# Kernel tuning notes

Hardware: AMD Instinct MI355X
Metric: run time of the kernel (lower is better)

## Reference

```python
import jax, jax.numpy as jnp
import numpy as np

B, IN, U = 16, 1024, 1024


def _wSw(W, S):
    # W: [i,u], S: [b,i,i] -> W^T S W : [b,u,u]
    return jnp.einsum('iu,bij,jv->buv', W, S, W)


def _xSx(x, Wsig):
    # (sum_i x_i^2) * W_Sigma, broadcast over batch
    return jnp.sum(x * x, axis=1)[:, None, None] * Wsig


def _trS(S, Wsig):
    return jnp.trace(S, axis1=1, axis2=2)[:, None, None] * Wsig


def _hadamard_sigma(s1, s2, m1, m2):
    # s1*s2 + diag(m1) s2 diag(m1) + diag(m2) s1 diag(m2)
    return (s1 * s2
            + m1[:, :, None] * s2 * m1[:, None, :]
            + m2[:, :, None] * s1 * m2[:, None, :])


def _act_sigma(g, S):
    # S * outer(g, g)
    return S * (g[:, :, None] * g[:, None, :])


def setup_inputs() -> dict:
    key = jax.random.key(0)
    ks = jax.random.split(key, 16)
    f32 = jnp.float32
    init_mu, ini_sigma = 0.05, -4.6
    inp = {
        'mu_inputs': jax.random.normal(ks[0], (B, IN), f32),
        'sigma_inputs': 0.01 * jax.random.normal(ks[1], (B, IN, IN), f32),
        'prev_state': 0.1 * jax.random.normal(ks[2], (B, U), f32),
        'Sigma_state': 0.01 * jax.random.normal(ks[3], (B, U, U), f32),
        'U_z': init_mu * jax.random.normal(ks[4], (IN, U), f32),
        'uz_sigma': jnp.full((U,), ini_sigma, f32),
        'W_z': init_mu * jax.random.normal(ks[5], (U, U), f32),
        'wz_sigma': jnp.full((U,), ini_sigma, f32),
        'U_r': init_mu * jax.random.normal(ks[6], (IN, U), f32),
        'ur_sigma': jnp.full((U,), ini_sigma, f32),
        'W_r': init_mu * jax.random.normal(ks[7], (U, U), f32),
        'wr_sigma': jnp.full((U,), ini_sigma, f32),
        'U_h': init_mu * jax.random.normal(ks[8], (IN, U), f32),
        'uh_sigma': jnp.full((U,), ini_sigma, f32),
        'W_h': init_mu * jax.random.normal(ks[9], (U, U), f32),
        'wh_sigma': jnp.full((U,), ini_sigma, f32),
    }
    return inp


def reference(mu_inputs, sigma_inputs, prev_state, Sigma_state,
              U_z, uz_sigma, W_z, wz_sigma,
              U_r, ur_sigma, W_r, wr_sigma,
              U_h, uh_sigma, W_h, wh_sigma):
    sp = jax.nn.softplus
    # ---- z gate ----
    pre_z = mu_inputs @ U_z + prev_state @ W_z
    z = jax.nn.sigmoid(pre_z)
    Uz_S, Wz_S = jnp.diag(sp(uz_sigma)), jnp.diag(sp(wz_sigma))
    Sigma_zz = (_wSw(U_z, sigma_inputs) + _xSx(mu_inputs, Uz_S) + _trS(sigma_inputs, Uz_S)
                + _wSw(W_z, Sigma_state) + _xSx(prev_state, Wz_S) + _trS(Sigma_state, Wz_S))
    Sigma_z = _act_sigma(z * (1.0 - z), Sigma_zz)  # analytic d sigmoid
    # ---- r gate ----
    pre_r = mu_inputs @ U_r + prev_state @ W_r
    r = jax.nn.sigmoid(pre_r)
    Ur_S, Wr_S = jnp.diag(sp(ur_sigma)), jnp.diag(sp(wr_sigma))
    Sigma_rr = (_wSw(U_r, sigma_inputs) + _xSx(mu_inputs, Ur_S) + _trS(sigma_inputs, Ur_S)
                + _wSw(W_r, Sigma_state) + _xSx(prev_state, Wr_S) + _trS(Sigma_state, Wr_S))
    Sigma_r = _act_sigma(r * (1.0 - r), Sigma_rr)
    # ---- h gate ----
    sr = prev_state * r
    pre_h = mu_inputs @ U_h + sr @ W_h
    h = jnp.tanh(pre_h)
    Uh_S, Wh_S = jnp.diag(sp(uh_sigma)), jnp.diag(sp(wh_sigma))
    sigma_g = _hadamard_sigma(Sigma_state, Sigma_r, prev_state, r)
    Sigma_hh = (_wSw(U_h, sigma_inputs) + _xSx(mu_inputs, Uh_S) + _trS(sigma_inputs, Uh_S)
                + _wSw(W_h, sigma_g) + _xSx(sr, Wh_S) + _trS(sigma_g, Wh_S))
    Sigma_h = _act_sigma(1.0 - h * h, Sigma_hh)  # analytic d tanh
    # ---- combine ----
    mu_out = z * prev_state + (1.0 - z) * h
    sigma_a = _hadamard_sigma(Sigma_z, Sigma_state, z, prev_state)
    sigma_b = _hadamard_sigma(Sigma_z, Sigma_h, 1.0 - z, h)
    sigma_ab = Sigma_z * (prev_state[:, :, None] * h[:, None, :])
    sigma_abT = Sigma_z * (h[:, :, None] * prev_state[:, None, :])
    Sigma_out = sigma_a + sigma_b - sigma_ab - sigma_abT
    Sigma_out = jnp.where(jnp.isfinite(Sigma_out), Sigma_out, jnp.zeros_like(Sigma_out))
    eye = jnp.eye(Sigma_out.shape[-1], dtype=bool)
    Sigma_out = jnp.where(eye, jnp.abs(Sigma_out), Sigma_out)
    return mu_out, Sigma_out
```

## Files before the change

### kernel.cpp

```cpp
#include <hip/hip_runtime.h>
#include <math.h>


#define B_  16
#define N_  1024
#define NN_ (1024*1024)

typedef __bf16 bf16x8 __attribute__((ext_vector_type(8)));
typedef float  f32x4  __attribute__((ext_vector_type(4)));
typedef unsigned short ushort8v __attribute__((ext_vector_type(8)));

__device__ __forceinline__ unsigned short f2bf(float f) {
  union { float f; unsigned int u; } v; v.f = f;
  unsigned int r = v.u + 0x7fffu + ((v.u >> 16) & 1u);
  return (unsigned short)(r >> 16);
}
__device__ __forceinline__ float bf2f(unsigned short h) {
  union { unsigned int u; float f; } v; v.u = ((unsigned int)h) << 16;
  return v.f;
}
__device__ __forceinline__ float f4get(const float4& v, int q) {
  return q == 0 ? v.x : (q == 1 ? v.y : (q == 2 ? v.z : v.w));
}
__device__ __forceinline__ unsigned short u4get(const ushort4& v, int q) {
  return q == 0 ? v.x : (q == 1 ? v.y : (q == 2 ? v.z : v.w));
}

__device__ __forceinline__ void gload_lds16(const void* g, void* l) {
  __builtin_amdgcn_global_load_lds((__attribute__((address_space(1))) void*)g,
                                   (__attribute__((address_space(3))) void*)l,
                                   16, 0, 0);
}

#define MFMA_ __builtin_amdgcn_mfma_f32_16x16x32_bf16
#define SBAR_()  do { __builtin_amdgcn_sched_barrier(0); \
                      __builtin_amdgcn_s_barrier(); \
                      __builtin_amdgcn_sched_barrier(0); } while (0)

template<int OMODE, int PAIR>
__global__ __launch_bounds__(512)
void gemm8p(const unsigned short* __restrict__ A, int lda, long aStride, int koffA,
            const unsigned short* __restrict__ Bm, const unsigned short* __restrict__ Bm2,
            int ldb, long bStride, int K,
            void* __restrict__ Out, int ldo, long oStride, int noff,
            const float* __restrict__ act,
            const float* __restrict__ spU, const float* __restrict__ spW,
            const float* __restrict__ dU, const float* __restrict__ dW)
{
  __shared__ __align__(16) char ldsb[131072];
  const int id = blockIdx.x;
  const int xcd = id & 7, rest = id >> 3;
  const int mt = rest & 3, pp = rest >> 2;
  const int panel = xcd + (pp << 3);
  const int nt = panel & 3;
  const int b  = (panel >> 2) & 15;
  const int ps = PAIR ? (panel >> 6) : 0;
  const unsigned short* Bsel = (PAIR && ps) ? Bm2 : Bm;
  const int kofx = koffA + (ps ? 1024 : 0);
  const int nofx = noff  + (ps ? 1024 : 0);
  const int mbase = mt << 8, nbase = nt << 8;
  const int tid = threadIdx.x, lane = tid & 63, w = tid >> 6;
  const int wm = w >> 2, wn = w & 3;
  const int NT = K >> 6;

  f32x4 acc[8][4];
  const f32x4 zero4 = {0.f, 0.f, 0.f, 0.f};
#pragma unroll
  for (int i = 0; i < 8; i++)
#pragma unroll
    for (int j = 0; j < 4; j++) acc[i][j] = zero4;

  const int l3 = lane >> 3, l7 = lane & 7;
  const int posg = l7 ^ l3;
  const int gr = (l3 << 1) + (posg >> 2);
  const int gc = (posg & 3) << 3;
  const int bi0 = w << 1, bi1 = bi0 + 1;
  const int rS0 = ((bi0 >> 1) << 4) + gr, cS0 = ((bi0 & 1) << 5) + gc;
  const int rS1 = ((bi1 >> 1) << 4) + gr, cS1 = ((bi1 & 1) << 5) + gc;
  const unsigned short* Ab = A + (size_t)b * aStride + (size_t)mbase * lda + kofx;
  const unsigned short* Bb = Bsel + (size_t)b * bStride + (size_t)nbase * ldb;
  const int d0 = w << 11, d1 = (w << 11) + 1024;

  auto SA = [&](int tt, int h) {
    char* dst = ldsb + ((tt & 1) << 16) + (h << 14);
    const unsigned short* s = Ab + (size_t)(h << 7) * lda + ((size_t)tt << 6);
    gload_lds16(s + (size_t)rS0 * lda + cS0, dst + d0);
    gload_lds16(s + (size_t)rS1 * lda + cS1, dst + d1);
  };
  auto SB = [&](int tt, int h) {
    char* dst = ldsb + ((tt & 1) << 16) + 32768 + (h << 14);
    const unsigned short* s = Bb + (size_t)(h << 7) * ldb + ((size_t)tt << 6);
    gload_lds16(s + (size_t)rS0 * ldb + cS0, dst + d0);
    gload_lds16(s + (size_t)rS1 * ldb + cS1, dst + d1);
  };

  const int lrow = lane & 15, c4 = lane >> 4;
  const int aoff = ((lrow >> 1) << 7) + (((((lrow & 1) << 2) | c4) ^ (lrow >> 1)) << 4);
  const int abase = wm << 14;
  const int bbase = 32768 + ((wn >> 1) << 14);
  const int brg   = (wn & 1) << 2;
  auto LDA = [&](const char* pb, int mi, int ks) -> bf16x8 {
    return *(const bf16x8*)(pb + abase + (((mi << 1) + ks) << 10) + aoff);
  };
  auto LDB = [&](const char* pb, int ni, int ks) -> bf16x8 {
    return *(const bf16x8*)(pb + bbase + ((((brg + ni) << 1) + ks) << 10) + aoff);
  };

  SA(0, 0); SA(0, 1); SB(0, 0); SB(0, 1);
  if (NT > 1) { SB(1, 0); SB(1, 1); }
  asm volatile("s_waitcnt vmcnt(4)" ::: "memory");
  SBAR_();

  bf16x8 avA[4], avB[4], bvA[4], bvB[4];
#pragma unroll
  for (int i = 0; i < 4; i++) avB[i] = LDA(ldsb, i, 0);
#pragma unroll
  for (int i = 0; i < 4; i++) bvB[i] = LDB(ldsb, i, 0);
  __builtin_amdgcn_sched_barrier(0);

  for (int kt = 0; kt < NT; ++kt) {
    const char* pb = ldsb + ((kt & 1) << 16);
    const char* pn = ldsb + (((kt + 1) & 1) << 16);
#pragma unroll
    for (int i = 0; i < 4; i++) avA[i] = LDA(pb, 4 + i, 0);
    if (kt + 1 < NT) SA(kt + 1, 0);
    SBAR_();
    __builtin_amdgcn_s_setprio(1);
#pragma unroll
    for (int ni = 0; ni < 4; ni++)
#pragma unroll
      for (int mi = 0; mi < 4; mi++)
        acc[mi][ni] = MFMA_(avB[mi], bvB[ni], acc[mi][ni], 0, 0, 0);
    __builtin_amdgcn_s_setprio(0);
    SBAR_();
#pragma unroll
    for (int i = 0; i < 4; i++) avB[i] = LDA(pb, i, 1);
#pragma unroll
    for (int i = 0; i < 4; i++) bvA[i] = LDB(pb, i, 1);
    if (kt + 1 < NT) SA(kt + 1, 1);
    SBAR_();
    __builtin_amdgcn_s_setprio(1);
#pragma unroll
    for (int ni = 0; ni < 4; ni++)
#pragma unroll
      for (int mi = 0; mi < 4; mi++)
        acc[4 + mi][ni] = MFMA_(avA[mi], bvB[ni], acc[4 + mi][ni], 0, 0, 0);
    __builtin_amdgcn_s_setprio(0);
    SBAR_();
#pragma unroll
    for (int i = 0; i < 4; i++) avA[i] = LDA(pb, 4 + i, 1);
    SBAR_();
    __builtin_amdgcn_s_setprio(1);
#pragma unroll
    for (int ni = 0; ni < 4; ni++)
#pragma unroll
      for (int mi = 0; mi < 4; mi++)
        acc[mi][ni] = MFMA_(avB[mi], bvA[ni], acc[mi][ni], 0, 0, 0);
    __builtin_amdgcn_s_setprio(0);
    SBAR_();
    if (kt + 2 < NT) {
      SB(kt + 2, 0); SB(kt + 2, 1);
      asm volatile("s_waitcnt vmcnt(4)" ::: "memory");
    } else if (kt + 1 < NT) {
      asm volatile("s_waitcnt vmcnt(0)" ::: "memory");
    }
    SBAR_();
    if (kt + 1 < NT) {
#pragma unroll
      for (int i = 0; i < 4; i++) avB[i] = LDA(pn, i, 0);
#pragma unroll
      for (int i = 0; i < 4; i++) bvB[i] = LDB(pn, i, 0);
    }
    __builtin_amdgcn_sched_barrier(0);
    __builtin_amdgcn_s_setprio(1);
#pragma unroll
    for (int ni = 0; ni < 4; ni++)
#pragma unroll
      for (int mi = 0; mi < 4; mi++)
        acc[4 + mi][ni] = MFMA_(avA[mi], bvA[ni], acc[4 + mi][ni], 0, 0, 0);
    __builtin_amdgcn_s_setprio(0);
    SBAR_();
  }

  if (OMODE == 2) {
    const float* actb = act + b * N_;
    const float dUb = dU[b], dWb = dW[b];
#pragma unroll
    for (int mi = 0; mi < 8; mi++) {
      const int u0 = mbase + wm * 128 + mi * 16 + ((lane >> 4) << 2);
#pragma unroll
      for (int ni = 0; ni < 4; ni++) {
        const int v = nbase + wn * 64 + ni * 16 + (lane & 15);
        const float avv = actb[v];
#pragma unroll
        for (int r = 0; r < 4; r++) {
          const int u = u0 + r;
          float val = acc[mi][ni][r];
          if (u == v) val += dUb * spU[u] + dWb * spW[u];
          val *= actb[u] * avv;
          ((float*)Out)[(size_t)b * oStride + (size_t)u * ldo + v] = val;
        }
      }
    }
  } else {
    __syncthreads();
    unsigned short* scr = (unsigned short*)(ldsb + w * 16384);
    const float* actb = (OMODE == 1) ? (act + b * N_) : nullptr;
    float dUb = 0.f, dWb = 0.f;
    if (OMODE == 1) { dUb = dU[b]; dWb = dW[b]; }
#pragma unroll
    for (int mi = 0; mi < 8; mi++) {
      const int rl0 = mi * 16 + ((lane >> 4) << 2);
#pragma unroll
      for (int ni = 0; ni < 4; ni++) {
        const int cl = ni * 16 + (lane & 15);
#pragma unroll
        for (int r = 0; r < 4; r++) {
          const int rl = rl0 + r;
          float val = acc[mi][ni][r];
          if (OMODE == 1) {
            const int u = mbase + wm * 128 + rl, v = nbase + wn * 64 + cl;
            if (u == v) val += dUb * spU[u] + dWb * spW[u];
            val *= actb[u] * actb[v];
          }
          scr[rl * 64 + ((((cl >> 3) ^ (rl & 7))) << 3) + (cl & 7)] = f2bf(val);
        }
      }
    }
    asm volatile("s_waitcnt lgkmcnt(0)" ::: "memory");
    __builtin_amdgcn_sched_barrier(0);
    unsigned short* ob = (unsigned short*)Out + (size_t)b * oStride
        + (size_t)(mbase + wm * 128) * ldo + nofx + nbase + wn * 64;
#pragma unroll
    for (int pq = 0; pq < 16; pq++) {
      const int row = pq * 8 + (lane >> 3);
      const int ch = (lane & 7) ^ (row & 7);
      ushort8v vv = *(const ushort8v*)&scr[row * 64 + ((lane & 7) << 3)];
      *(ushort8v*)(ob + (size_t)row * ldo + ch * 8) = vv;
    }
  }
}


__global__ void conv_bf16(const float* __restrict__ in, unsigned short* __restrict__ out, int n4)
{
  int i = blockIdx.x * 256 + threadIdx.x;
  const int stride = gridDim.x * 256;
  for (; i < n4; i += stride) {
    const float4 v = ((const float4*)in)[i];
    ushort4 o;
    o.x = f2bf(v.x); o.y = f2bf(v.y); o.z = f2bf(v.z); o.w = f2bf(v.w);
    ((ushort4*)out)[i] = o;
  }
}

__global__ void build_AT(const float* __restrict__ Uz, const float* __restrict__ Wz,
                         const float* __restrict__ Ur, const float* __restrict__ Wr,
                         const float* __restrict__ Uh, const float* __restrict__ Wh,
                         unsigned short* __restrict__ AT)
{
  __shared__ float tile[32][33];
  const int g = blockIdx.z;
  const float* U = g == 0 ? Uz : (g == 1 ? Ur : Uh);
  const float* W = g == 0 ? Wz : (g == 1 ? Wr : Wh);
  const int u0  = blockIdx.x * 32;
  const int k0g = blockIdx.y * 32;
  const float* src = (k0g >= 1024) ? W : U;
  const int kloc = k0g & 1023;
  const int tx = threadIdx.x & 31, ty = threadIdx.x >> 5;
  unsigned short* out = AT + (size_t)g * N_ * 2048;
#pragma unroll
  for (int i = 0; i < 32; i += 8) tile[ty + i][tx] = src[(size_t)(kloc + ty + i) * N_ + u0 + tx];
  __syncthreads();
#pragma unroll
  for (int i = 0; i < 32; i += 8)
    out[(size_t)(u0 + ty + i) * 2048 + k0g + tx] = f2bf(tile[tx][ty + i]);
}

__global__ void softplus6(const float* a0, const float* a1, const float* a2,
                          const float* a3, const float* a4, const float* a5,
                          float* __restrict__ sp)
{
  const float* src[6] = {a0, a1, a2, a3, a4, a5};
  const int g = blockIdx.x;
  const float* s = src[g];
  for (int i = threadIdx.x; i < N_; i += 256) {
    float x = s[i];
    sp[g * N_ + i] = (x > 20.f) ? x : log1pf(expf(x));
  }
}

__global__ void scalars1(const float* __restrict__ mu, const float* __restrict__ prev,
                         const float* __restrict__ sin_, const float* __restrict__ Sst,
                         float* __restrict__ dA, float* __restrict__ dBzr)
{
  __shared__ float red[256];
  const int b = blockIdx.x;
  float s1 = 0.f, s2 = 0.f;
  for (int i = threadIdx.x; i < N_; i += 256) {
    const float m = mu[b * N_ + i];
    s1 += m * m + sin_[(size_t)b * NN_ + (size_t)i * (N_ + 1)];
    const float p = prev[b * N_ + i];
    s2 += p * p + Sst[(size_t)b * NN_ + (size_t)i * (N_ + 1)];
  }
  red[threadIdx.x] = s1; __syncthreads();
  for (int s = 128; s > 0; s >>= 1) { if (threadIdx.x < s) red[threadIdx.x] += red[threadIdx.x + s]; __syncthreads(); }
  if (threadIdx.x == 0) dA[b] = red[0];
  __syncthreads();
  red[threadIdx.x] = s2; __syncthreads();
  for (int s = 128; s > 0; s >>= 1) { if (threadIdx.x < s) red[threadIdx.x] += red[threadIdx.x + s]; __syncthreads(); }
  if (threadIdx.x == 0) dBzr[b] = red[0];
}

__global__ __launch_bounds__(256)
void gate_pre2(const float* __restrict__ x1, const float* __restrict__ x2,
               const float* __restrict__ U0, const float* __restrict__ W0,
               const float* __restrict__ U1, const float* __restrict__ W1,
               float* __restrict__ Ppart)
{
  const int g  = blockIdx.z;
  const int ks = blockIdx.y;
  const int out = blockIdx.x * 256 + threadIdx.x;
  const int b = out >> 10, col = out & 1023;
  const float* x = (ks < 4) ? x1 : x2;
  const float* Wm = (g == 0) ? ((ks < 4) ? U0 : W0) : ((ks < 4) ? U1 : W1);
  const int k0 = (ks & 3) * 256;
  const float* xb = x + b * N_ + k0;
  const float* wp = Wm + (size_t)k0 * N_ + col;
  float acc = 0.f;
#pragma unroll 8
  for (int k = 0; k < 256; k++)
    acc += xb[k] * wp[(size_t)k * N_];
  Ppart[(g * 8 + ks) * (B_ * N_) + out] = acc;
}

__global__ void gate_act2(const float* __restrict__ P,
                          float* __restrict__ z, float* __restrict__ gz,
                          float* __restrict__ r, float* __restrict__ gr)
{
  const int out = blockIdx.x * 256 + threadIdx.x;
  float a0 = 0.f, a1 = 0.f;
#pragma unroll
  for (int ks = 0; ks < 8; ks++) {
    a0 += P[ks * (B_ * N_) + out];
    a1 += P[(8 + ks) * (B_ * N_) + out];
  }
  const float s0 = 1.f / (1.f + expf(-a0));
  const float s1 = 1.f / (1.f + expf(-a1));
  z[out] = s0; gz[out] = s0 * (1.f - s0);
  r[out] = s1; gr[out] = s1 * (1.f - s1);
}

__global__ __launch_bounds__(256)
void gate_pre1(const float* __restrict__ x1, const float* __restrict__ x2,
               const float* __restrict__ U0, const float* __restrict__ W0,
               float* __restrict__ Ppart)
{
  const int ks = blockIdx.y;
  const int out = blockIdx.x * 256 + threadIdx.x;
  const int b = out >> 10, col = out & 1023;
  const float* x = (ks < 4) ? x1 : x2;
  const float* Wm = (ks < 4) ? U0 : W0;
  const int k0 = (ks & 3) * 256;
  const float* xb = x + b * N_ + k0;
  const float* wp = Wm + (size_t)k0 * N_ + col;
  float acc = 0.f;
#pragma unroll 8
  for (int k = 0; k < 256; k++)
    acc += xb[k] * wp[(size_t)k * N_];
  Ppart[ks * (B_ * N_) + out] = acc;
}

__global__ void gate_act1(const float* __restrict__ P,
                          float* __restrict__ h, float* __restrict__ gh)
{
  const int out = blockIdx.x * 256 + threadIdx.x;
  float a0 = 0.f;
#pragma unroll
  for (int ks = 0; ks < 8; ks++) a0 += P[ks * (B_ * N_) + out];
  const float s = tanhf(a0);
  h[out] = s; gh[out] = 1.f - s * s;
}

__global__ void sr_csr(const float* __restrict__ prev, const float* __restrict__ r,
                       float* __restrict__ sr, float* __restrict__ csr)
{
  __shared__ float red[256];
  const int b = blockIdx.x;
  float s = 0.f;
  for (int i = threadIdx.x; i < N_; i += 256) {
    const float v = prev[b * N_ + i] * r[b * N_ + i];
    sr[b * N_ + i] = v;
    s += v * v;
  }
  red[threadIdx.x] = s; __syncthreads();
  for (int k = 128; k > 0; k >>= 1) { if (threadIdx.x < k) red[threadIdx.x] += red[threadIdx.x + k]; __syncthreads(); }
  if (threadIdx.x == 0) csr[b] = red[0];
}

__global__ void hadamard_sg(const float* __restrict__ Sst, unsigned short* __restrict__ Sg,
                            const float* __restrict__ prev, const float* __restrict__ r)
{
  const size_t idx = ((size_t)blockIdx.x * 256 + threadIdx.x) * 4;
  const int b = (int)(idx >> 20);
  const int rem = (int)(idx & (NN_ - 1));
  const int i = rem >> 10, j0 = rem & 1023;
  const float pi = prev[b * N_ + i], ri = r[b * N_ + i];
  const float4  ss  = *(const float4*)(Sst + (size_t)b * NN_ + rem);
  const ushort4 sr4 = *(const ushort4*)(Sg + (size_t)b * NN_ + rem);
  ushort4 o;
  unsigned short* op = (unsigned short*)&o;
#pragma unroll
  for (int q = 0; q < 4; q++) {
    const float srv = bf2f(u4get(sr4, q));
    const float stv = f4get(ss, q);
    const float pj = prev[b * N_ + j0 + q];
    const float rj = r[b * N_ + j0 + q];
    op[q] = f2bf(stv * srv + pi * pj * srv + ri * rj * stv);
  }
  *(ushort4*)(Sg + (size_t)b * NN_ + rem) = o;
}

__global__ void scalars2(const unsigned short* __restrict__ Sg,
                         const float* __restrict__ csr, float* __restrict__ dBh)
{
  __shared__ float red[256];
  const int b = blockIdx.x;
  float s = 0.f;
  for (int i = threadIdx.x; i < N_; i += 256)
    s += bf2f(Sg[(size_t)b * NN_ + (size_t)i * (N_ + 1)]);
  red[threadIdx.x] = s; __syncthreads();
  for (int k = 128; k > 0; k >>= 1) { if (threadIdx.x < k) red[threadIdx.x] += red[threadIdx.x + k]; __syncthreads(); }
  if (threadIdx.x == 0) dBh[b] = red[0] + csr[b];
}

__global__ void mu_kernel(const float* __restrict__ z, const float* __restrict__ prev,
                          const float* __restrict__ h, float* __restrict__ mu_out)
{
  const int i = blockIdx.x * 256 + threadIdx.x;
  const float zz = z[i];
  mu_out[i] = zz * prev[i] + (1.f - zz) * h[i];
}

__global__ void combine(const unsigned short* __restrict__ Sz, const float* __restrict__ Sst,
                        const float* __restrict__ z, const float* __restrict__ prev,
                        const float* __restrict__ h, float* __restrict__ SigOut)
{
  const int row = blockIdx.x;
  const int b = row >> 10, u = row & 1023;
  const float zu = z[b * N_ + u], pu = prev[b * N_ + u], hu = h[b * N_ + u];
  const size_t base = (size_t)b * NN_ + (size_t)u * N_;
  const int j0 = threadIdx.x * 4;
  const ushort4 s4 = *(const ushort4*)(Sz + base + j0);
  const float4 sh = *(const float4*)(SigOut + base + j0);
  const float4 st = *(const float4*)(Sst + base + j0);
  const float4 zv = *(const float4*)(z + b * N_ + j0);
  const float4 pv = *(const float4*)(prev + b * N_ + j0);
  const float4 hv = *(const float4*)(h + b * N_ + j0);
  float o[4];
#pragma unroll
  for (int q = 0; q < 4; q++) {
    const int v = j0 + q;
    const float sz  = bf2f(u4get(s4, q));
    const float shh = f4get(sh, q);
    const float stt = f4get(st, q);
    const float zvv = f4get(zv, q);
    const float pvv = f4get(pv, q);
    const float hvv = f4get(hv, q);
    float res = sz * stt + zu * zvv * stt + pu * pvv * sz
              + sz * shh + (1.f - zu) * (1.f - zvv) * shh + hu * hvv * sz
              - sz * (pu * hvv) - sz * (hu * pvv);
    if (!isfinite(res)) res = 0.f;
    if (u == v) res = fabsf(res);
    o[q] = res;
  }
  float4 ov; ov.x = o[0]; ov.y = o[1]; ov.z = o[2]; ov.w = o[3];
  *(float4*)(SigOut + base + j0) = ov;
}


extern "C" void kernel_launch(void* const* d_in, const int* in_sizes, int n_in,
                              void* d_out, int out_size, void* d_ws, size_t ws_size,
                              hipStream_t stream)
{
  const float* mu   = (const float*)d_in[0];
  const float* sin_ = (const float*)d_in[1];
  const float* prev = (const float*)d_in[2];
  const float* Sst  = (const float*)d_in[3];
  const float* Uz = (const float*)d_in[4];  const float* uzs = (const float*)d_in[5];
  const float* Wz = (const float*)d_in[6];  const float* wzs = (const float*)d_in[7];
  const float* Ur = (const float*)d_in[8];  const float* urs = (const float*)d_in[9];
  const float* Wr = (const float*)d_in[10]; const float* wrs = (const float*)d_in[11];
  const float* Uh = (const float*)d_in[12]; const float* uhs = (const float*)d_in[13];
  const float* Wh = (const float*)d_in[14]; const float* whs = (const float*)d_in[15];

  char* ws = (char*)d_ws;
  size_t off = 0;
  auto take = [&](size_t bytes) -> char* {
    char* p = ws + off;
    off = (off + bytes + 255) & ~(size_t)255;
    return p;
  };
  unsigned short* Tcm = (unsigned short*)take((size_t)B_ * 2048 * 1024 * 2);
  unsigned short* Sz  = (unsigned short*)take((size_t)B_ * NN_ * 2);
  unsigned short* Sg  = (unsigned short*)take((size_t)B_ * NN_ * 2);
  unsigned short* AT  = (unsigned short*)take((size_t)3 * N_ * 2048 * 2);
  float* Ppart = (float*)take((size_t)16 * B_ * N_ * 4);
  float* sp   = (float*)take(6 * N_ * 4);
  float* z    = (float*)take(B_ * N_ * 4);
  float* gz   = (float*)take(B_ * N_ * 4);
  float* rr   = (float*)take(B_ * N_ * 4);
  float* gr   = (float*)take(B_ * N_ * 4);
  float* h    = (float*)take(B_ * N_ * 4);
  float* gh   = (float*)take(B_ * N_ * 4);
  float* sr   = (float*)take(B_ * N_ * 4);
  float* dA   = (float*)take(64);
  float* dBzr = (float*)take(64);
  float* dBh  = (float*)take(64);
  float* csr  = (float*)take(64);
  if (off > ws_size) return;

  float* mu_out = (float*)d_out;
  float* SigOut = (float*)d_out + (size_t)B_ * N_;
  unsigned short* SinH = (unsigned short*)SigOut;
  unsigned short* SstH = (unsigned short*)SigOut + (size_t)B_ * NN_;

  const unsigned short* ATz = AT;
  const unsigned short* ATr = AT + (size_t)N_ * 2048;
  const unsigned short* ATh = AT + (size_t)2 * N_ * 2048;

  conv_bf16<<<2048, 256, 0, stream>>>(sin_, SinH, B_ * NN_ / 4);
  conv_bf16<<<2048, 256, 0, stream>>>(Sst,  SstH, B_ * NN_ / 4);
  softplus6<<<6, 256, 0, stream>>>(uzs, wzs, urs, wrs, uhs, whs, sp);
  scalars1<<<16, 256, 0, stream>>>(mu, prev, sin_, Sst, dA, dBzr);
  build_AT<<<dim3(32, 64, 3), 256, 0, stream>>>(Uz, Wz, Ur, Wr, Uh, Wh, AT);
  gate_pre2<<<dim3(64, 8, 2), 256, 0, stream>>>(mu, prev, Uz, Wz, Ur, Wr, Ppart);
  gate_act2<<<64, 256, 0, stream>>>(Ppart, z, gz, rr, gr);
  sr_csr<<<16, 256, 0, stream>>>(prev, rr, sr, csr);
  gate_pre1<<<dim3(64, 8), 256, 0, stream>>>(mu, sr, Uh, Wh, Ppart);
  gate_act1<<<64, 256, 0, stream>>>(Ppart, h, gh);

  const long tS = (long)2048 * 1024;

  gemm8p<0, 1><<<512, 512, 0, stream>>>(ATz, 2048, 0, 0, SinH, SstH, 1024, (long)NN_, 1024,
                                        Tcm, 2048, tS, 0, nullptr, nullptr, nullptr, nullptr, nullptr);
  gemm8p<1, 0><<<256, 512, 0, stream>>>(ATz, 2048, 0, 0, Tcm, nullptr, 2048, tS, 2048,
                                        Sz, 1024, (long)NN_, 0, gz, sp + 0, sp + 1024, dA, dBzr);
  gemm8p<0, 1><<<512, 512, 0, stream>>>(ATr, 2048, 0, 0, SinH, SstH, 1024, (long)NN_, 1024,
                                        Tcm, 2048, tS, 0, nullptr, nullptr, nullptr, nullptr, nullptr);
  gemm8p<1, 0><<<256, 512, 0, stream>>>(ATr, 2048, 0, 0, Tcm, nullptr, 2048, tS, 2048,
                                        Sg, 1024, (long)NN_, 0, gr, sp + 2048, sp + 3072, dA, dBzr);
  hadamard_sg<<<16384, 256, 0, stream>>>(Sst, Sg, prev, rr);
  scalars2<<<16, 256, 0, stream>>>(Sg, csr, dBh);
  gemm8p<0, 1><<<512, 512, 0, stream>>>(ATh, 2048, 0, 0, SinH, Sg, 1024, (long)NN_, 1024,
                                        Tcm, 2048, tS, 0, nullptr, nullptr, nullptr, nullptr, nullptr);
  gemm8p<2, 0><<<256, 512, 0, stream>>>(ATh, 2048, 0, 0, Tcm, nullptr, 2048, tS, 2048,
                                        SigOut, 1024, (long)NN_, 0, gh, sp + 4096, sp + 5120, dA, dBh);
  mu_kernel<<<64, 256, 0, stream>>>(z, prev, h, mu_out);
  combine<<<16384, 256, 0, stream>>>(Sz, Sst, z, prev, h, SigOut);
}
```

Measured before the change: 574.7 us.

## Fuse final combine into last GEMM epilogue and merge small elementwise kernels

The separate combine kernel is removed, and its Hadamard combination of Sz, Sigma_state, z, prev and h is computed directly in the OMODE==2 GEMM epilogue. This avoids writing Sigma_hh to the output and reading it back. The mu_out computation moves into gate_act1, the two bf16 conversions become one launch, and hadamard_sg reads the bf16 copy of Sigma_state instead of fp32. The epilogue stores are still scalar with strided per-lane access and now load Sz and Sst per element. The bf16 Sigma_state in hadamard_sg slightly lowers precision.

```diff
diff --git a/kernel.cpp b/kernel.cpp
--- a/kernel.cpp
+++ b/kernel.cpp
@@ -45,7 +45,10 @@
             void* __restrict__ Out, int ldo, long oStride, int noff,
             const float* __restrict__ act,
             const float* __restrict__ spU, const float* __restrict__ spW,
-            const float* __restrict__ dU, const float* __restrict__ dW)
+            const float* __restrict__ dU, const float* __restrict__ dW,
+            const unsigned short* __restrict__ SzP, const float* __restrict__ SstP,
+            const float* __restrict__ zV, const float* __restrict__ prevV,
+            const float* __restrict__ hV)
 {
   __shared__ __align__(16) char ldsb[131072];
   const int id = blockIdx.x;
@@ -183,22 +186,43 @@
   }
 
   if (OMODE == 2) {
-    const float* actb = act + b * N_;
+    const float* ghb = act + b * N_;
     const float dUb = dU[b], dWb = dW[b];
+    const float* zb = zV + b * N_;
+    const float* pv = prevV + b * N_;
+    const float* hb = hV + b * N_;
+    const unsigned short* SzB = SzP + (size_t)b * NN_;
+    const float* SstB = SstP + (size_t)b * NN_;
+    float zvv[4], pvv[4], hvv[4], gvv[4];
+    int vcol[4];
+#pragma unroll
+    for (int ni = 0; ni < 4; ni++) {
+      const int v = nbase + wn * 64 + ni * 16 + (lane & 15);
+      vcol[ni] = v;
+      zvv[ni] = zb[v]; pvv[ni] = pv[v]; hvv[ni] = hb[v]; gvv[ni] = ghb[v];
+    }
 #pragma unroll
     for (int mi = 0; mi < 8; mi++) {
       const int u0 = mbase + wm * 128 + mi * 16 + ((lane >> 4) << 2);
 #pragma unroll
-      for (int ni = 0; ni < 4; ni++) {
-        const int v = nbase + wn * 64 + ni * 16 + (lane & 15);
-        const float avv = actb[v];
-#pragma unroll
-        for (int r = 0; r < 4; r++) {
-          const int u = u0 + r;
-          float val = acc[mi][ni][r];
-          if (u == v) val += dUb * spU[u] + dWb * spW[u];
-          val *= actb[u] * avv;
-          ((float*)Out)[(size_t)b * oStride + (size_t)u * ldo + v] = val;
+      for (int r = 0; r < 4; r++) {
+        const int u = u0 + r;
+        const float zu = zb[u], pu = pv[u], hu = hb[u], gu = ghb[u];
+        const float diag = dUb * spU[u] + dWb * spW[u];
+#pragma unroll
+        for (int ni = 0; ni < 4; ni++) {
+          const int v = vcol[ni];
+          float shh = acc[mi][ni][r];
+          if (u == v) shh += diag;
+          shh *= gu * gvv[ni];
+          const float szv = bf2f(SzB[(size_t)u * N_ + v]);
+          const float stt = SstB[(size_t)u * N_ + v];
+          float res = szv * stt + zu * zvv[ni] * stt + pu * pvv[ni] * szv
+                    + szv * shh + (1.f - zu) * (1.f - zvv[ni]) * shh + hu * hvv[ni] * szv
+                    - szv * (pu * hvv[ni]) - szv * (hu * pvv[ni]);
+          if (!isfinite(res)) res = 0.f;
+          if (u == v) res = fabsf(res);
+          ((float*)Out)[(size_t)b * oStride + (size_t)u * ldo + v] = res;
         }
       }
     }
@@ -242,8 +266,12 @@
 }
 
 
-__global__ void conv_bf16(const float* __restrict__ in, unsigned short* __restrict__ out, int n4)
-{
+__global__ void conv_bf16_2(const float* __restrict__ in0, unsigned short* __restrict__ out0,
+                            const float* __restrict__ in1, unsigned short* __restrict__ out1,
+                            int n4)
+{
+  const float* in = blockIdx.y ? in1 : in0;
+  unsigned short* out = blockIdx.y ? out1 : out0;
   int i = blockIdx.x * 256 + threadIdx.x;
   const int stride = gridDim.x * 256;
   for (; i < n4; i += stride) {
@@ -372,7 +400,9 @@
 }
 
 __global__ void gate_act1(const float* __restrict__ P,
-                          float* __restrict__ h, float* __restrict__ gh)
+                          const float* __restrict__ z, const float* __restrict__ prev,
+                          float* __restrict__ h, float* __restrict__ gh,
+                          float* __restrict__ mu_out)
 {
   const int out = blockIdx.x * 256 + threadIdx.x;
   float a0 = 0.f;
@@ -380,6 +410,8 @@
   for (int ks = 0; ks < 8; ks++) a0 += P[ks * (B_ * N_) + out];
   const float s = tanhf(a0);
   h[out] = s; gh[out] = 1.f - s * s;
+  const float zz = z[out];
+  mu_out[out] = zz * prev[out] + (1.f - zz) * s;
 }
 
 __global__ void sr_csr(const float* __restrict__ prev, const float* __restrict__ r,
@@ -398,7 +430,8 @@
   if (threadIdx.x == 0) csr[b] = red[0];
 }
 
-__global__ void hadamard_sg(const float* __restrict__ Sst, unsigned short* __restrict__ Sg,
+__global__ void hadamard_sg(const unsigned short* __restrict__ SstH,
+                            unsigned short* __restrict__ Sg,
                             const float* __restrict__ prev, const float* __restrict__ r)
 {
   const size_t idx = ((size_t)blockIdx.x * 256 + threadIdx.x) * 4;
@@ -406,14 +439,14 @@
   const int rem = (int)(idx & (NN_ - 1));
   const int i = rem >> 10, j0 = rem & 1023;
   const float pi = prev[b * N_ + i], ri = r[b * N_ + i];
-  const float4  ss  = *(const float4*)(Sst + (size_t)b * NN_ + rem);
+  const ushort4 ss4 = *(const ushort4*)(SstH + (size_t)b * NN_ + rem);
   const ushort4 sr4 = *(const ushort4*)(Sg + (size_t)b * NN_ + rem);
   ushort4 o;
   unsigned short* op = (unsigned short*)&o;
 #pragma unroll
   for (int q = 0; q < 4; q++) {
     const float srv = bf2f(u4get(sr4, q));
-    const float stv = f4get(ss, q);
+    const float stv = bf2f(u4get(ss4, q));
     const float pj = prev[b * N_ + j0 + q];
     const float rj = r[b * N_ + j0 + q];
     op[q] = f2bf(stv * srv + pi * pj * srv + ri * rj * stv);
@@ -432,50 +465,6 @@
   red[threadIdx.x] = s; __syncthreads();
   for (int k = 128; k > 0; k >>= 1) { if (threadIdx.x < k) red[threadIdx.x] += red[threadIdx.x + k]; __syncthreads(); }
   if (threadIdx.x == 0) dBh[b] = red[0] + csr[b];
-}
-
-__global__ void mu_kernel(const float* __restrict__ z, const float* __restrict__ prev,
-                          const float* __restrict__ h, float* __restrict__ mu_out)
-{
-  const int i = blockIdx.x * 256 + threadIdx.x;
-  const float zz = z[i];
-  mu_out[i] = zz * prev[i] + (1.f - zz) * h[i];
-}
-
-__global__ void combine(const unsigned short* __restrict__ Sz, const float* __restrict__ Sst,
-                        const float* __restrict__ z, const float* __restrict__ prev,
-                        const float* __restrict__ h, float* __restrict__ SigOut)
-{
-  const int row = blockIdx.x;
-  const int b = row >> 10, u = row & 1023;
-  const float zu = z[b * N_ + u], pu = prev[b * N_ + u], hu = h[b * N_ + u];
-  const size_t base = (size_t)b * NN_ + (size_t)u * N_;
-  const int j0 = threadIdx.x * 4;
-  const ushort4 s4 = *(const ushort4*)(Sz + base + j0);
-  const float4 sh = *(const float4*)(SigOut + base + j0);
-  const float4 st = *(const float4*)(Sst + base + j0);
-  const float4 zv = *(const float4*)(z + b * N_ + j0);
-  const float4 pv = *(const float4*)(prev + b * N_ + j0);
-  const float4 hv = *(const float4*)(h + b * N_ + j0);
-  float o[4];
-#pragma unroll
-  for (int q = 0; q < 4; q++) {
-    const int v = j0 + q;
-    const float sz  = bf2f(u4get(s4, q));
-    const float shh = f4get(sh, q);
-    const float stt = f4get(st, q);
-    const float zvv = f4get(zv, q);
-    const float pvv = f4get(pv, q);
-    const float hvv = f4get(hv, q);
-    float res = sz * stt + zu * zvv * stt + pu * pvv * sz
-              + sz * shh + (1.f - zu) * (1.f - zvv) * shh + hu * hvv * sz
-              - sz * (pu * hvv) - sz * (hu * pvv);
-    if (!isfinite(res)) res = 0.f;
-    if (u == v) res = fabsf(res);
-    o[q] = res;
-  }
-  float4 ov; ov.x = o[0]; ov.y = o[1]; ov.z = o[2]; ov.w = o[3];
-  *(float4*)(SigOut + base + j0) = ov;
 }
 
 
@@ -529,8 +518,7 @@
   const unsigned short* ATr = AT + (size_t)N_ * 2048;
   const unsigned short* ATh = AT + (size_t)2 * N_ * 2048;
 
-  conv_bf16<<<2048, 256, 0, stream>>>(sin_, SinH, B_ * NN_ / 4);
-  conv_bf16<<<2048, 256, 0, stream>>>(Sst,  SstH, B_ * NN_ / 4);
+  conv_bf16_2<<<dim3(2048, 2), 256, 0, stream>>>(sin_, SinH, Sst, SstH, B_ * NN_ / 4);
   softplus6<<<6, 256, 0, stream>>>(uzs, wzs, urs, wrs, uhs, whs, sp);
   scalars1<<<16, 256, 0, stream>>>(mu, prev, sin_, Sst, dA, dBzr);
   build_AT<<<dim3(32, 64, 3), 256, 0, stream>>>(Uz, Wz, Ur, Wr, Uh, Wh, AT);
@@ -538,24 +526,28 @@
   gate_act2<<<64, 256, 0, stream>>>(Ppart, z, gz, rr, gr);
   sr_csr<<<16, 256, 0, stream>>>(prev, rr, sr, csr);
   gate_pre1<<<dim3(64, 8), 256, 0, stream>>>(mu, sr, Uh, Wh, Ppart);
-  gate_act1<<<64, 256, 0, stream>>>(Ppart, h, gh);
+  gate_act1<<<64, 256, 0, stream>>>(Ppart, z, prev, h, gh, mu_out);
 
   const long tS = (long)2048 * 1024;
 
   gemm8p<0, 1><<<512, 512, 0, stream>>>(ATz, 2048, 0, 0, SinH, SstH, 1024, (long)NN_, 1024,
-                                        Tcm, 2048, tS, 0, nullptr, nullptr, nullptr, nullptr, nullptr);
+                                        Tcm, 2048, tS, 0, nullptr, nullptr, nullptr, nullptr, nullptr,
+                                        nullptr, nullptr, nullptr, nullptr, nullptr);
   gemm8p<1, 0><<<256, 512, 0, stream>>>(ATz, 2048, 0, 0, Tcm, nullptr, 2048, tS, 2048,
-                                        Sz, 1024, (long)NN_, 0, gz, sp + 0, sp + 1024, dA, dBzr);
+                                        Sz, 1024, (long)NN_, 0, gz, sp + 0, sp + 1024, dA, dBzr,
+                                        nullptr, nullptr, nullptr, nullptr, nullptr);
   gemm8p<0, 1><<<512, 512, 0, stream>>>(ATr, 2048, 0, 0, SinH, SstH, 1024, (long)NN_, 1024,
-                                        Tcm, 2048, tS, 0, nullptr, nullptr, nullptr, nullptr, nullptr);
+                                        Tcm, 2048, tS, 0, nullptr, nullptr, nullptr, nullptr, nullptr,
+                                        nullptr, nullptr, nullptr, nullptr, nullptr);
   gemm8p<1, 0><<<256, 512, 0, stream>>>(ATr, 2048, 0, 0, Tcm, nullptr, 2048, tS, 2048,
-                                        Sg, 1024, (long)NN_, 0, gr, sp + 2048, sp + 3072, dA, dBzr);
-  hadamard_sg<<<16384, 256, 0, stream>>>(Sst, Sg, prev, rr);
+                                        Sg, 1024, (long)NN_, 0, gr, sp + 2048, sp + 3072, dA, dBzr,
+                                        nullptr, nullptr, nullptr, nullptr, nullptr);
+  hadamard_sg<<<16384, 256, 0, stream>>>(SstH, Sg, prev, rr);
   scalars2<<<16, 256, 0, stream>>>(Sg, csr, dBh);
   gemm8p<0, 1><<<512, 512, 0, stream>>>(ATh, 2048, 0, 0, SinH, Sg, 1024, (long)NN_, 1024,
-                                        Tcm, 2048, tS, 0, nullptr, nullptr, nullptr, nullptr, nullptr);
+                                        Tcm, 2048, tS, 0, nullptr, nullptr, nullptr, nullptr, nullptr,
+                                        nullptr, nullptr, nullptr, nullptr, nullptr);
   gemm8p<2, 0><<<256, 512, 0, stream>>>(ATh, 2048, 0, 0, Tcm, nullptr, 2048, tS, 2048,
-                                        SigOut, 1024, (long)NN_, 0, gh, sp + 4096, sp + 5120, dA, dBh);
-  mu_kernel<<<64, 256, 0, stream>>>(z, prev, h, mu_out);
-  combine<<<16384, 256, 0, stream>>>(Sz, Sst, z, prev, h, SigOut);
-}
+                                        SigOut, 1024, (long)NN_, 0, gh, sp + 4096, sp + 5120, dA, dBh,
+                                        Sz, Sst, z, prev, h);
+}
```

Result: faster. 547.8 us (-4.7%).
